# Kernel optimization log

Hardware: AMD Instinct MI355X
Metric: run time of the kernel (lower is better)

Reference implementation:

```python
import jax, jax.numpy as jnp
import numpy as np

RNN = 512
ENC = 512
HID = 512
ATT_SIZE = 196
B = 1024


def setup_inputs() -> dict:
    key = jax.random.key(0)
    ks = jax.random.split(key, 20)
    s = 0.02
    d = {
        "h": jax.random.normal(ks[0], (B, RNN), jnp.float32),
        "sentinel": jax.random.normal(ks[1], (B, RNN), jnp.float32),
        "att_feats": jax.random.normal(ks[2], (B, ATT_SIZE, RNN), jnp.float32),
        "W_ctx2att": jax.random.normal(ks[3], (RNN, HID), jnp.float32) * s,
        "b_ctx2att": jnp.zeros((HID,), jnp.float32),
        "W_sl": jax.random.normal(ks[4], (RNN, ENC), jnp.float32) * s,
        "b_sl": jnp.zeros((ENC,), jnp.float32),
        "W_se": jax.random.normal(ks[5], (ENC, HID), jnp.float32) * s,
        "b_se": jnp.zeros((HID,), jnp.float32),
        "W_hl": jax.random.normal(ks[6], (RNN, ENC), jnp.float32) * s,
        "b_hl": jnp.zeros((ENC,), jnp.float32),
        "W_he": jax.random.normal(ks[7], (ENC, HID), jnp.float32) * s,
        "b_he": jnp.zeros((HID,), jnp.float32),
        "W_alpha": jax.random.normal(ks[8], (HID, 1), jnp.float32) * s,
        "b_alpha": jnp.zeros((1,), jnp.float32),
        "W_att2h": jax.random.normal(ks[9], (RNN, RNN), jnp.float32) * s,
        "b_att2h": jnp.zeros((RNN,), jnp.float32),
    }
    return d


def reference(h, sentinel, att_feats, W_ctx2att, b_ctx2att, W_sl, b_sl,
              W_se, b_se, W_hl, b_hl, W_he, b_he, W_alpha, b_alpha,
              W_att2h, b_att2h):
    # Eval mode: dropout is identity.
    # Project attention features: [B, 196, HID]
    p_att = jnp.einsum("bsd,dh->bsh", att_feats, W_ctx2att) + b_ctx2att
    # Sentinel branch
    sent_lin = jax.nn.relu(sentinel @ W_sl + b_sl)          # [B, ENC]
    sent_emb = sent_lin @ W_se + b_se                       # [B, HID]
    # Hidden-state branch
    h_lin = jnp.tanh(h @ W_hl + b_hl)                       # [B, ENC]
    h_emb = h_lin @ W_he + b_he                             # [B, HID]
    # Concat sentinel with visual features: [B, 197, *]
    img_all = jnp.concatenate([sent_lin[:, None, :], att_feats], axis=1)
    img_all_embed = jnp.concatenate([sent_emb[:, None, :], p_att], axis=1)
    # Additive attention scores over 197 positions
    hA = jnp.tanh(img_all_embed + h_emb[:, None, :])        # [B, 197, HID]
    scores = (jnp.einsum("bsh,ho->bso", hA, W_alpha) + b_alpha)[..., 0]  # [B, 197]
    alpha = jax.nn.softmax(scores, axis=-1)
    # Weighted context
    cHat = jnp.einsum("bs,bsd->bd", alpha, img_all)          # [B, RNN]
    atten_out = cHat + h_lin
    out = jnp.tanh(atten_out @ W_att2h + b_att2h)            # [B, RNN]
    return out
```

## Files before the change

### kernel.cpp

```cpp
#include <hip/hip_runtime.h>
#include <hip/hip_bf16.h>

#define KDIM 512
#define NDIM 512
#define ATT  196
#define NB   1024

typedef __attribute__((ext_vector_type(8))) short bf16x8;
typedef __attribute__((ext_vector_type(8))) unsigned short ushort8;
typedef __attribute__((ext_vector_type(4))) float f32x4;

typedef const __attribute__((address_space(1))) unsigned int gas_uint;
typedef __attribute__((address_space(3))) unsigned int las_uint;

__device__ __forceinline__ void gload16(const void* g, void* l) {
    __builtin_amdgcn_global_load_lds((gas_uint*)g, (las_uint*)l, 16, 0, 0);
}

__device__ __forceinline__ float fast_tanh(float x) {
    x = fminf(15.f, fmaxf(-15.f, x));
    float t = __expf(2.f * x);
    return (t - 1.f) / (t + 1.f);
}

__device__ __forceinline__ unsigned short f2bf(float x) {
    union { float f; unsigned u; } v; v.f = x;
    unsigned r = v.u + 0x7FFF + ((v.u >> 16) & 1);
    return (unsigned short)(r >> 16);
}

__device__ __forceinline__ unsigned pk2(float a, float b) {
    unsigned r;
    asm("v_cvt_pk_bf16_f32 %0, %1, %2" : "=v"(r) : "v"(a), "v"(b));
    return r;
}

__global__ __launch_bounds__(256) void prep_weights(
        const float* __restrict__ W0, const float* __restrict__ W1,
        const float* __restrict__ W2, const float* __restrict__ W3,
        const float* __restrict__ W4, const float* __restrict__ W5,
        unsigned short* __restrict__ Wt) {
    int w = blockIdx.x >> 6;
    int t = blockIdx.x & 63;
    int k0 = (t >> 3) << 6, n0 = (t & 7) << 6;
    const float* W = (w == 0) ? W0 : (w == 1) ? W1 : (w == 2) ? W2 :
                     (w == 3) ? W3 : (w == 4) ? W4 : W5;
    __shared__ float tile[64][65];
    int tid = threadIdx.x;
    int nc = tid & 15, kr = tid >> 4;
#pragma unroll
    for (int i = 0; i < 4; ++i) {
        int k = kr + i * 16;
        float4 v = *(const float4*)&W[(size_t)(k0 + k) * NDIM + n0 + nc * 4];
        tile[k][nc * 4 + 0] = v.x; tile[k][nc * 4 + 1] = v.y;
        tile[k][nc * 4 + 2] = v.z; tile[k][nc * 4 + 3] = v.w;
    }
    __syncthreads();
    int n = tid >> 2, ks = tid & 3;
    ushort8 v0, v1;
#pragma unroll
    for (int j = 0; j < 8; ++j) v0[j] = f2bf(tile[ks * 16 + j][n]);
#pragma unroll
    for (int j = 0; j < 8; ++j) v1[j] = f2bf(tile[ks * 16 + 8 + j][n]);
    size_t base = ((size_t)w << 18) + (size_t)(n0 + n) * KDIM + k0 + ks * 16;
    *(ushort8*)&Wt[base] = v0;
    *(ushort8*)&Wt[base + 8] = v1;
}

__global__ __launch_bounds__(256) void gemm64(
        const float* __restrict__ A0, const unsigned short* __restrict__ W0,
        const float* __restrict__ bia0, float* __restrict__ O0, int act0,
        const float* __restrict__ A1, const unsigned short* __restrict__ W1,
        const float* __restrict__ bia1, float* __restrict__ O1, int act1) {
    const int op = blockIdx.y;
    const float* A = op ? A1 : A0;
    const unsigned short* Bt = op ? W1 : W0;
    const float* bias = op ? bia1 : bia0;
    float* out = op ? O1 : O0;
    const int act = op ? act1 : act0;

    __shared__ unsigned short A_lds[2][64 * 32];
    __shared__ unsigned short B_lds[2][128 * 32];

    const int tid = threadIdx.x;
    const int gm0 = (blockIdx.x >> 2) * 64, gn0 = (blockIdx.x & 3) * 128;
    const int wid = tid >> 6, lane = tid & 63;
    const int wm = wid >> 1, wn = wid & 1;
    const int lr = lane & 15, lk = lane >> 4;

    const int arow = tid >> 2, akc = tid & 3;
    const float* aptr = A + (size_t)(gm0 + arow) * KDIM + akc * 8;
    const int aoff = arow * 32 + ((akc ^ ((arow >> 1) & 3)) << 3);

    auto stageB = [&](int kt, int buf) {
#pragma unroll
        for (int j = 0; j < 2; ++j) {
            int c = tid + j * 256;
            int col = c >> 2, slot = c & 3;
            const unsigned short* src = Bt + (size_t)(gn0 + col) * KDIM +
                                        ((slot ^ ((col >> 1) & 3)) << 3) + kt * 32;
            gload16(src, &B_lds[buf][c * 8]);
        }
    };

    f32x4 acc[2][4] = {};

    {
        float4 x0 = *(const float4*)aptr;
        float4 x1 = *(const float4*)(aptr + 4);
        stageB(0, 0);
        uint4 p;
        p.x = pk2(x0.x, x0.y); p.y = pk2(x0.z, x0.w);
        p.z = pk2(x1.x, x1.y); p.w = pk2(x1.z, x1.w);
        *(uint4*)&A_lds[0][aoff] = p;
    }
    __syncthreads();

    const int swk = ((lk ^ ((lr >> 1) & 3)) << 3);
    for (int kt = 0; kt < 16; ++kt) {
        const int buf = kt & 1;
        float4 x0, x1;
        if (kt < 15) {
            const float* ap = aptr + (kt + 1) * 32;
            x0 = *(const float4*)ap;
            x1 = *(const float4*)(ap + 4);
            stageB(kt + 1, buf ^ 1);
        }
        bf16x8 af[2], bfr[4];
#pragma unroll
        for (int m = 0; m < 2; ++m)
            af[m] = *(const bf16x8*)&A_lds[buf][(wm * 32 + m * 16 + lr) * 32 + swk];
#pragma unroll
        for (int n = 0; n < 4; ++n)
            bfr[n] = *(const bf16x8*)&B_lds[buf][(wn * 64 + n * 16 + lr) * 32 + swk];
#pragma unroll
        for (int m = 0; m < 2; ++m)
#pragma unroll
            for (int n = 0; n < 4; ++n)
                acc[m][n] = __builtin_amdgcn_mfma_f32_16x16x32_bf16(af[m], bfr[n], acc[m][n], 0, 0, 0);
        if (kt < 15) {
            uint4 p;
            p.x = pk2(x0.x, x0.y); p.y = pk2(x0.z, x0.w);
            p.z = pk2(x1.x, x1.y); p.w = pk2(x1.z, x1.w);
            *(uint4*)&A_lds[buf ^ 1][aoff] = p;
        }
        __syncthreads();
    }

#pragma unroll
    for (int m = 0; m < 2; ++m)
#pragma unroll
        for (int n = 0; n < 4; ++n) {
            int col = gn0 + wn * 64 + n * 16 + lr;
            float bsv = bias[col];
#pragma unroll
            for (int r = 0; r < 4; ++r) {
                int row = gm0 + wm * 32 + m * 16 + lk * 4 + r;
                float v = acc[m][n][r] + bsv;
                if (act == 0) v = fmaxf(v, 0.f);
                else if (act == 1) v = fast_tanh(v);
                out[(size_t)row * NDIM + col] = v;
            }
        }
}

__launch_bounds__(512, 4)
__global__ void gemm_score(const float* __restrict__ A,
                           const unsigned short* __restrict__ Bt,
                           const float* __restrict__ b_ctx,
                           const float* __restrict__ h_emb,
                           const float* __restrict__ Walpha,
                           float* __restrict__ score) {
    __shared__ char smem[81920];
    float (*A_f)[256 * 32] = (float (*)[256 * 32])smem;
    unsigned short (*B_lds)[128 * 32] = (unsigned short (*)[128 * 32])(smem + 65536);
    float* ch_s = (float*)smem;
    float* wa_s = (float*)(smem + 1536);
    float* s_red = (float*)(smem + 2048);

    const int tid  = threadIdx.x;
    const int bidx = blockIdx.x;
    const int xcd  = bidx & 7, u = bidx >> 3;
    const int mblk = xcd * 98 + (u >> 2), nblk = u & 3;
    const int gm0  = mblk * 256, gn0 = nblk * 128;

    const int wid = tid >> 6, lane = tid & 63;
    const int wm  = wid >> 1, wn = wid & 1;
    const int lr  = lane & 15, lk = lane >> 4;

    const float* asrc[4];
#pragma unroll
    for (int i = 0; i < 4; ++i) {
        int c = tid + i * 512;
        int row = c >> 3, g = c & 7;
        asrc[i] = A + (size_t)(gm0 + row) * KDIM + ((g ^ (row & 7)) << 2);
    }
    auto stageA = [&](int kt, int buf) {
#pragma unroll
        for (int i = 0; i < 4; ++i)
            gload16(asrc[i] + kt * 32, &A_f[buf][(tid + i * 512) * 4]);
    };

    const int bcol = tid >> 2, bslot = tid & 3;
    const unsigned short* bsrc = Bt + (size_t)(gn0 + bcol) * KDIM +
                                 ((bslot ^ ((bcol >> 1) & 3)) << 3);
    auto stageB = [&](int kt, int buf) {
        gload16(bsrc + kt * 32, &B_lds[buf][tid * 8]);
    };

    f32x4 acc[4][4] = {};
    const int swk = ((lk ^ ((lr >> 1) & 3)) << 3);
    const int arw = lr & 7;
    const int as0 = (lk * 2) ^ arw;
    const int as1 = (lk * 2 + 1) ^ arw;

    stageA(0, 0);
    stageB(0, 0);
    __syncthreads();

#pragma unroll 1
    for (int kt = 0; kt < 16; ++kt) {
        const int buf = kt & 1;
        if (kt < 15) {
            stageA(kt + 1, buf ^ 1);
            stageB(kt + 1, buf ^ 1);
        }
        bf16x8 af[4], bfr[4];
#pragma unroll
        for (int n = 0; n < 4; ++n)
            bfr[n] = *(const bf16x8*)&B_lds[buf][(wn * 64 + n * 16 + lr) * 32 + swk];
#pragma unroll
        for (int m = 0; m < 4; ++m) {
            const int rbase = (wm * 64 + m * 16 + lr) * 32;
            float4 fa = *(const float4*)&A_f[buf][rbase + as0 * 4];
            float4 fb = *(const float4*)&A_f[buf][rbase + as1 * 4];
            uint4 p;
            p.x = pk2(fa.x, fa.y); p.y = pk2(fa.z, fa.w);
            p.z = pk2(fb.x, fb.y); p.w = pk2(fb.z, fb.w);
            union { uint4 u; bf16x8 v; } cc; cc.u = p;
            af[m] = cc.v;
        }
#pragma unroll
        for (int m = 0; m < 4; ++m)
#pragma unroll
            for (int n = 0; n < 4; ++n)
                acc[m][n] = __builtin_amdgcn_mfma_f32_16x16x32_bf16(af[m], bfr[n], acc[m][n], 0, 0, 0);
        __syncthreads();
    }

    const int bb0 = gm0 / ATT;
    {
        int j = tid >> 7;
        int c = tid & 127;
        if (j < 3) {
            int bb = bb0 + j; if (bb > NB - 1) bb = NB - 1;
            ch_s[j * 128 + c] = b_ctx[gn0 + c] + h_emb[(size_t)bb * NDIM + gn0 + c];
        }
        if (tid < 128) wa_s[tid] = Walpha[gn0 + tid];
    }
    __syncthreads();

#pragma unroll
    for (int m = 0; m < 4; ++m) {
#pragma unroll
        for (int r = 0; r < 4; ++r) {
            int rloc = wm * 64 + m * 16 + lk * 4 + r;
            int rg = gm0 + rloc;
            int sel = rg / ATT - bb0;
            float sum = 0.f;
#pragma unroll
            for (int n = 0; n < 4; ++n) {
                int cloc = wn * 64 + n * 16 + lr;
                sum += fast_tanh(acc[m][n][r] + ch_s[sel * 128 + cloc]) * wa_s[cloc];
            }
            sum += __shfl_xor(sum, 1);
            sum += __shfl_xor(sum, 2);
            sum += __shfl_xor(sum, 4);
            sum += __shfl_xor(sum, 8);
            if (lr == 0) s_red[wn * 256 + rloc] = sum;
        }
    }
    __syncthreads();
    if (tid < 256) {
        float tot = s_red[tid] + s_red[256 + tid];
        int rg = gm0 + tid;
        int bb = rg / ATT;
        atomicAdd(&score[(size_t)bb * 197 + (rg - bb * ATT) + 1], tot);
    }
}

__global__ __launch_bounds__(256) void softmax_chat(
        const float* __restrict__ score, const float* __restrict__ sent_emb,
        const float* __restrict__ h_emb, const float* __restrict__ Walpha,
        const float* __restrict__ sent_lin, const float* __restrict__ h_lin,
        const float* __restrict__ att, float* __restrict__ atten_out) {
    int b = blockIdx.x, tid = threadIdx.x;
    __shared__ float al[200];
    __shared__ float r4[4];

    float2 se = ((const float2*)(sent_emb + (size_t)b * NDIM))[tid];
    float2 he = ((const float2*)(h_emb + (size_t)b * NDIM))[tid];
    float2 wa = ((const float2*)Walpha)[tid];
    float val = fast_tanh(se.x + he.x) * wa.x + fast_tanh(se.y + he.y) * wa.y;
#pragma unroll
    for (int o = 32; o; o >>= 1) val += __shfl_xor(val, o);
    if ((tid & 63) == 0) r4[tid >> 6] = val;
    __syncthreads();
    float ssent = r4[0] + r4[1] + r4[2] + r4[3];
    __syncthreads();

    float v = -1e30f;
    if (tid < 197) v = (tid == 0) ? ssent : score[(size_t)b * 197 + tid];
    float m = v;
#pragma unroll
    for (int o = 32; o; o >>= 1) m = fmaxf(m, __shfl_xor(m, o));
    if ((tid & 63) == 0) r4[tid >> 6] = m;
    __syncthreads();
    m = fmaxf(fmaxf(r4[0], r4[1]), fmaxf(r4[2], r4[3]));
    __syncthreads();
    float e = (tid < 197) ? __expf(v - m) : 0.f;
    float s = e;
#pragma unroll
    for (int o = 32; o; o >>= 1) s += __shfl_xor(s, o);
    if ((tid & 63) == 0) r4[tid >> 6] = s;
    __syncthreads();
    s = r4[0] + r4[1] + r4[2] + r4[3];
    if (tid < 197) al[tid] = e / s;
    __syncthreads();

    const float2* af = (const float2*)(att + (size_t)b * ATT * KDIM);
    float2 a0 = ((const float2*)(sent_lin + (size_t)b * KDIM))[tid];
    float w0 = al[0];
    float2 accv; accv.x = w0 * a0.x; accv.y = w0 * a0.y;
#pragma unroll 14
    for (int ss = 0; ss < ATT; ++ss) {
        float w = al[ss + 1];
        float2 x = af[(size_t)ss * 256 + tid];
        accv.x += w * x.x; accv.y += w * x.y;
    }
    float2 hl = ((const float2*)(h_lin + (size_t)b * KDIM))[tid];
    accv.x += hl.x; accv.y += hl.y;
    ((float2*)(atten_out + (size_t)b * KDIM))[tid] = accv;
}

extern "C" void kernel_launch(void* const* d_in, const int* in_sizes, int n_in,
                              void* d_out, int out_size, void* d_ws, size_t ws_size,
                              hipStream_t stream) {
    const float* h     = (const float*)d_in[0];
    const float* sent  = (const float*)d_in[1];
    const float* att   = (const float*)d_in[2];
    const float* W_ctx = (const float*)d_in[3];
    const float* b_ctx = (const float*)d_in[4];
    const float* W_sl  = (const float*)d_in[5];
    const float* b_sl  = (const float*)d_in[6];
    const float* W_se  = (const float*)d_in[7];
    const float* b_se  = (const float*)d_in[8];
    const float* W_hl  = (const float*)d_in[9];
    const float* b_hl  = (const float*)d_in[10];
    const float* W_he  = (const float*)d_in[11];
    const float* b_he  = (const float*)d_in[12];
    const float* W_al  = (const float*)d_in[13];
    const float* W_a2h = (const float*)d_in[15];
    const float* b_a2h = (const float*)d_in[16];
    float* out = (float*)d_out;

    char* ws = (char*)d_ws;
    unsigned short* Wt = (unsigned short*)ws;
    float* sent_lin = (float*)(ws + 6u * 512 * 1024);
    float* h_lin    = sent_lin + (size_t)NB * 512;
    float* h_emb    = h_lin    + (size_t)NB * 512;
    float* sent_emb = h_emb    + (size_t)NB * 512;
    float* scorebuf = sent_emb + (size_t)NB * 512;
    float* atten    = scorebuf + (size_t)NB * 197;

    const size_t WSZ = 512 * 512;
    prep_weights<<<384, 256, 0, stream>>>(W_sl, W_hl, W_he, W_ctx, W_a2h, W_se, Wt);
    hipMemsetAsync(scorebuf, 0, (size_t)NB * 197 * sizeof(float), stream);

    gemm64<<<dim3(64, 2), 256, 0, stream>>>(
        sent, Wt + 0 * WSZ, b_sl, sent_lin, 0,
        h,    Wt + 1 * WSZ, b_hl, h_lin,    1);
    gemm64<<<dim3(64, 2), 256, 0, stream>>>(
        h_lin,    Wt + 2 * WSZ, b_he, h_emb,    2,
        sent_lin, Wt + 5 * WSZ, b_se, sent_emb, 2);

    gemm_score<<<3136, 512, 0, stream>>>(att, Wt + 3 * WSZ, b_ctx, h_emb, W_al, scorebuf);

    softmax_chat<<<NB, 256, 0, stream>>>(scorebuf, sent_emb, h_emb, W_al,
                                         sent_lin, h_lin, att, atten);

    gemm64<<<dim3(64, 1), 256, 0, stream>>>(
        atten, Wt + 4 * WSZ, b_a2h, out, 1,
        atten, Wt + 4 * WSZ, b_a2h, out, 1);
}
```

Baseline: 362.1 us.

## Convert A tile to bf16 once in registers before LDS store in score GEMM

The A operand of the score GEMM was copied into LDS as fp32 with direct global-to-LDS loads and converted to bf16 by every wave reading it. It is now loaded into registers, packed to bf16 once, and written to a swizzled bf16 LDS buffer after the MFMAs of each step, with reads done via single bf16x8 loads. This shrinks LDS from 80KB to 48KB, which allows more blocks per CU, and removes redundant conversions across the waves sharing a tile. The cost is register-staged global loads that no longer bypass VGPRs, plus a store issued before the barrier, which may expose global latency.

```diff
diff --git a/kernel.cpp b/kernel.cpp
--- a/kernel.cpp
+++ b/kernel.cpp
@@ -171,9 +171,9 @@
                            const float* __restrict__ h_emb,
                            const float* __restrict__ Walpha,
                            float* __restrict__ score) {
-    __shared__ char smem[81920];
-    float (*A_f)[256 * 32] = (float (*)[256 * 32])smem;
-    unsigned short (*B_lds)[128 * 32] = (unsigned short (*)[128 * 32])(smem + 65536);
+    __shared__ char smem[49152];
+    unsigned short (*A_lds)[256 * 32] = (unsigned short (*)[256 * 32])smem;
+    unsigned short (*B_lds)[128 * 32] = (unsigned short (*)[128 * 32])(smem + 32768);
     float* ch_s = (float*)smem;
     float* wa_s = (float*)(smem + 1536);
     float* s_red = (float*)(smem + 2048);
@@ -188,18 +188,11 @@
     const int wm  = wid >> 1, wn = wid & 1;
     const int lr  = lane & 15, lk = lane >> 4;
 
-    const float* asrc[4];
-#pragma unroll
-    for (int i = 0; i < 4; ++i) {
-        int c = tid + i * 512;
-        int row = c >> 3, g = c & 7;
-        asrc[i] = A + (size_t)(gm0 + row) * KDIM + ((g ^ (row & 7)) << 2);
-    }
-    auto stageA = [&](int kt, int buf) {
-#pragma unroll
-        for (int i = 0; i < 4; ++i)
-            gload16(asrc[i] + kt * 32, &A_f[buf][(tid + i * 512) * 4]);
-    };
+    const int arow = tid >> 1, ahalf = tid & 1;
+    const float* aptr = A + (size_t)(gm0 + arow) * KDIM + ahalf * 16;
+    const int skc0  = (ahalf * 2) ^ ((arow >> 1) & 3);
+    const int aoff0 = arow * 32 + skc0 * 8;
+    const int aoff1 = arow * 32 + (skc0 ^ 1) * 8;
 
     const int bcol = tid >> 2, bslot = tid & 3;
     const unsigned short* bsrc = Bt + (size_t)(gn0 + bcol) * KDIM +
@@ -207,22 +200,40 @@
     auto stageB = [&](int kt, int buf) {
         gload16(bsrc + kt * 32, &B_lds[buf][tid * 8]);
     };
+    auto writeA = [&](const float4& x0, const float4& x1,
+                      const float4& x2, const float4& x3, int buf) {
+        uint4 p0, p1;
+        p0.x = pk2(x0.x, x0.y); p0.y = pk2(x0.z, x0.w);
+        p0.z = pk2(x1.x, x1.y); p0.w = pk2(x1.z, x1.w);
+        p1.x = pk2(x2.x, x2.y); p1.y = pk2(x2.z, x2.w);
+        p1.z = pk2(x3.x, x3.y); p1.w = pk2(x3.z, x3.w);
+        *(uint4*)&A_lds[buf][aoff0] = p0;
+        *(uint4*)&A_lds[buf][aoff1] = p1;
+    };
 
     f32x4 acc[4][4] = {};
     const int swk = ((lk ^ ((lr >> 1) & 3)) << 3);
-    const int arw = lr & 7;
-    const int as0 = (lk * 2) ^ arw;
-    const int as1 = (lk * 2 + 1) ^ arw;
-
-    stageA(0, 0);
-    stageB(0, 0);
+
+    {
+        float4 x0 = *(const float4*)(aptr);
+        float4 x1 = *(const float4*)(aptr + 4);
+        float4 x2 = *(const float4*)(aptr + 8);
+        float4 x3 = *(const float4*)(aptr + 12);
+        stageB(0, 0);
+        writeA(x0, x1, x2, x3, 0);
+    }
     __syncthreads();
 
 #pragma unroll 1
     for (int kt = 0; kt < 16; ++kt) {
         const int buf = kt & 1;
+        float4 x0, x1, x2, x3;
         if (kt < 15) {
-            stageA(kt + 1, buf ^ 1);
+            const float* ap = aptr + (kt + 1) * 32;
+            x0 = *(const float4*)(ap);
+            x1 = *(const float4*)(ap + 4);
+            x2 = *(const float4*)(ap + 8);
+            x3 = *(const float4*)(ap + 12);
             stageB(kt + 1, buf ^ 1);
         }
         bf16x8 af[4], bfr[4];
@@ -230,21 +241,14 @@
         for (int n = 0; n < 4; ++n)
             bfr[n] = *(const bf16x8*)&B_lds[buf][(wn * 64 + n * 16 + lr) * 32 + swk];
 #pragma unroll
-        for (int m = 0; m < 4; ++m) {
-            const int rbase = (wm * 64 + m * 16 + lr) * 32;
-            float4 fa = *(const float4*)&A_f[buf][rbase + as0 * 4];
-            float4 fb = *(const float4*)&A_f[buf][rbase + as1 * 4];
-            uint4 p;
-            p.x = pk2(fa.x, fa.y); p.y = pk2(fa.z, fa.w);
-            p.z = pk2(fb.x, fb.y); p.w = pk2(fb.z, fb.w);
-            union { uint4 u; bf16x8 v; } cc; cc.u = p;
-            af[m] = cc.v;
-        }
+        for (int m = 0; m < 4; ++m)
+            af[m] = *(const bf16x8*)&A_lds[buf][(wm * 64 + m * 16 + lr) * 32 + swk];
 #pragma unroll
         for (int m = 0; m < 4; ++m)
 #pragma unroll
             for (int n = 0; n < 4; ++n)
                 acc[m][n] = __builtin_amdgcn_mfma_f32_16x16x32_bf16(af[m], bfr[n], acc[m][n], 0, 0, 0);
+        if (kt < 15) writeA(x0, x1, x2, x3, buf ^ 1);
         __syncthreads();
     }
 
```

After: 361.3 us. No clear change (-0.2%).
